# Performance work log

Hardware: AMD Instinct MI355X
Metric: run time of the kernel (lower is better)

## Reference

```python
import jax, jax.numpy as jnp
import numpy as np

N_NODES = 100000
N_EDGES = 3200000
D_IN = 128
D_OUT = 128


def setup_inputs() -> dict:
    key = jax.random.key(0)
    k1, k2, k3 = jax.random.split(key, 3)
    x = jax.random.normal(k1, (N_NODES, D_IN), dtype=jnp.float32)
    edge_index = jax.random.randint(k2, (2, N_EDGES), 0, N_NODES, dtype=jnp.int64)
    # Glorot-style init for GCN weight
    W = jax.random.normal(k3, (D_IN, D_OUT), dtype=jnp.float32) * (1.0 / np.sqrt(D_IN))
    b = jnp.zeros((D_OUT,), dtype=jnp.float32)
    return {"x": x, "edge_index": edge_index, "W": W, "b": b}


def reference(x, edge_index, W, b):
    # GCNConv (PyG semantics): add self-loops, symmetric normalization
    # D^-1/2 A D^-1/2, linear transform, aggregate, add bias; then ReLU.
    N = x.shape[0]
    loops = jnp.arange(N, dtype=edge_index.dtype)
    row = jnp.concatenate([edge_index[0], loops])  # source nodes
    col = jnp.concatenate([edge_index[1], loops])  # target nodes
    # degree over targets, with self-loop weight 1
    deg = jax.ops.segment_sum(jnp.ones_like(col, dtype=x.dtype), col,
                              num_segments=N)
    dinv = jnp.where(deg > 0, 1.0 / jnp.sqrt(deg), 0.0)
    norm = dinv[row] * dinv[col]                   # [E+N]
    xl = x @ W                                     # [N, D_OUT] dense GEMM
    msgs = xl[row] * norm[:, None]                 # gather + scale  [E+N, D_OUT]
    agg = jax.ops.segment_sum(msgs, col, num_segments=N)  # scatter-add
    return jax.nn.relu(agg + b)
```

## Files before the change

### kernel.cpp

```cpp
#include <hip/hip_runtime.h>
#include <hip/hip_bf16.h>
#include <math.h>

#define DF 128
#define TILE_EDGES 16384
#define NPB 256
#define NB_MAX 512

typedef __hip_bfloat16 bf16;
typedef __hip_bfloat162 bf16x2;

__global__ __launch_bounds__(1024) void k_binc(const int* __restrict__ col,
                                               int* __restrict__ counts,
                                               int E, int T, int NB) {
    __shared__ int h[NB_MAX];
    int tid = threadIdx.x;
    for (int i = tid; i < NB; i += 1024) h[i] = 0;
    __syncthreads();
    int tileBase = blockIdx.x * TILE_EDGES;
    for (int j = 0; j < TILE_EDGES / 1024; ++j) {
        int e = tileBase + j * 1024 + tid;
        if (e < E) atomicAdd(&h[col[e] >> 8], 1);
    }
    __syncthreads();
    for (int b = tid; b < NB; b += 1024)
        counts[b * T + blockIdx.x] = h[b];
}

__global__ __launch_bounds__(256) void k_scanA(int* __restrict__ data,
                                               int* __restrict__ blockSums, int M) {
    __shared__ int tmp[256];
    int tid = threadIdx.x;
    int n = blockIdx.x * 256 + tid;
    int v = (n < M) ? data[n] : 0;
    tmp[tid] = v;
    __syncthreads();
    for (int off = 1; off < 256; off <<= 1) {
        int t = (tid >= off) ? tmp[tid - off] : 0;
        __syncthreads();
        tmp[tid] += t;
        __syncthreads();
    }
    if (tid == 255) blockSums[blockIdx.x] = tmp[255];
    if (n < M) data[n] = tmp[tid] - v;
}

__global__ __launch_bounds__(512) void k_scanB(int* __restrict__ blockSums, int nb) {
    __shared__ int tmp[512];
    int tid = threadIdx.x;
    int v = (tid < nb) ? blockSums[tid] : 0;
    tmp[tid] = v;
    __syncthreads();
    for (int off = 1; off < 512; off <<= 1) {
        int t = (tid >= off) ? tmp[tid - off] : 0;
        __syncthreads();
        tmp[tid] += t;
        __syncthreads();
    }
    if (tid < nb) blockSums[tid] = tmp[tid] - v;
}

__global__ __launch_bounds__(256) void k_scanC(int* __restrict__ data,
                                               const int* __restrict__ blockSums,
                                               int* __restrict__ bucketBase,
                                               int M, int T, int NB, int E) {
    int n = blockIdx.x * 256 + threadIdx.x;
    if (n >= M) return;
    int v = data[n] + blockSums[n >> 8];
    data[n] = v;
    if (n % T == 0) bucketBase[n / T] = v;
    if (n == 0) bucketBase[NB] = E;
}

__global__ __launch_bounds__(1024) void k_binscatter(const int* __restrict__ edge,
                                                     const int* __restrict__ tileOff,
                                                     unsigned* __restrict__ binned,
                                                     int E, int T, int NB) {
    __shared__ int cur[NB_MAX];
    int tid = threadIdx.x;
    int t = blockIdx.x;
    for (int b = tid; b < NB; b += 1024) cur[b] = tileOff[b * T + t];
    __syncthreads();
    int tileBase = t * TILE_EDGES;
    for (int j = 0; j < TILE_EDGES / 1024; ++j) {
        int e = tileBase + j * 1024 + tid;
        if (e < E) {
            int r = edge[e];
            int c = edge[E + e];
            int pos = atomicAdd(&cur[c >> 8], 1);
            binned[pos] = ((unsigned)(c & (NPB - 1)) << 24) | (unsigned)r;
        }
    }
}

__global__ __launch_bounds__(512) void k_bucket(const unsigned* __restrict__ binned,
                                                const int* __restrict__ bucketBase,
                                                int* __restrict__ ssrc,
                                                int* __restrict__ offsets,
                                                int* __restrict__ deg,
                                                float* __restrict__ dinv, int N) {
    __shared__ int h[NPB], sc[NPB], cur[NPB];
    int tid = threadIdx.x;
    int b = blockIdx.x;
    int base = bucketBase[b];
    int cnt = bucketBase[b + 1] - base;
    if (tid < NPB) h[tid] = 0;
    __syncthreads();
    for (int i = tid; i < cnt; i += 512)
        atomicAdd(&h[binned[base + i] >> 24], 1);
    __syncthreads();
    if (tid < NPB) sc[tid] = h[tid];
    __syncthreads();
    for (int off = 1; off < NPB; off <<= 1) {
        int tv = (tid >= off && tid < NPB) ? sc[tid - off] : 0;
        __syncthreads();
        if (tid < NPB) sc[tid] += tv;
        __syncthreads();
    }
    if (tid < NPB) {
        int excl = sc[tid] - h[tid];
        cur[tid] = base + excl;
        int node = b * NPB + tid;
        if (node < N) {
            offsets[node] = base + excl;
            deg[node] = h[tid];
            dinv[node] = rsqrtf((float)(h[tid] + 1));
        }
    }
    __syncthreads();
    for (int i = tid; i < cnt; i += 512) {
        unsigned v = binned[base + i];
        int pos = atomicAdd(&cur[v >> 24], 1);
        ssrc[pos] = (int)(v & 0xFFFFFFu);
    }
}

__device__ inline void fma4(float4& acc, const float4 xv, const float4 w0,
                            const float4 w1, const float4 w2, const float4 w3) {
    acc.x = fmaf(xv.x, w0.x, fmaf(xv.y, w1.x, fmaf(xv.z, w2.x, fmaf(xv.w, w3.x, acc.x))));
    acc.y = fmaf(xv.x, w0.y, fmaf(xv.y, w1.y, fmaf(xv.z, w2.y, fmaf(xv.w, w3.y, acc.y))));
    acc.z = fmaf(xv.x, w0.z, fmaf(xv.y, w1.z, fmaf(xv.z, w2.z, fmaf(xv.w, w3.z, acc.z))));
    acc.w = fmaf(xv.x, w0.w, fmaf(xv.y, w1.w, fmaf(xv.z, w2.w, fmaf(xv.w, w3.w, acc.w))));
}

__device__ inline uint2 pack_bf16x4(float4 a) {
    union { uint2 u; bf16x2 h[2]; } p;
    p.h[0] = __float22bfloat162_rn(make_float2(a.x, a.y));
    p.h[1] = __float22bfloat162_rn(make_float2(a.z, a.w));
    return p.u;
}

__global__ __launch_bounds__(256) void k_gemm(const float* __restrict__ x,
                                              const float* __restrict__ W,
                                              const float* __restrict__ dinv,
                                              bf16* __restrict__ y, int N) {
    __shared__ float Ws[DF * DF];
    for (int i = threadIdx.x; i < DF * DF / 4; i += 256)
        ((float4*)Ws)[i] = ((const float4*)W)[i];
    __syncthreads();

    const int fg = (threadIdx.x & 31) * 4;
    const int rl = (threadIdx.x >> 5) * 4;

    for (int rowBase = blockIdx.x * 32; rowBase < N; rowBase += gridDim.x * 32) {
        int r0 = rowBase + rl;
        int c0 = min(r0 + 0, N - 1), c1 = min(r0 + 1, N - 1);
        int c2 = min(r0 + 2, N - 1), c3 = min(r0 + 3, N - 1);
        const float4* x0 = (const float4*)(x + (size_t)c0 * DF);
        const float4* x1 = (const float4*)(x + (size_t)c1 * DF);
        const float4* x2 = (const float4*)(x + (size_t)c2 * DF);
        const float4* x3 = (const float4*)(x + (size_t)c3 * DF);
        float4 a0 = {0, 0, 0, 0}, a1 = {0, 0, 0, 0}, a2 = {0, 0, 0, 0}, a3 = {0, 0, 0, 0};
        for (int k4 = 0; k4 < DF / 4; ++k4) {
            float4 xv0 = x0[k4], xv1 = x1[k4], xv2 = x2[k4], xv3 = x3[k4];
            int k = k4 * 4;
            float4 w0 = *(const float4*)(Ws + (k + 0) * DF + fg);
            float4 w1 = *(const float4*)(Ws + (k + 1) * DF + fg);
            float4 w2 = *(const float4*)(Ws + (k + 2) * DF + fg);
            float4 w3 = *(const float4*)(Ws + (k + 3) * DF + fg);
            fma4(a0, xv0, w0, w1, w2, w3);
            fma4(a1, xv1, w0, w1, w2, w3);
            fma4(a2, xv2, w0, w1, w2, w3);
            fma4(a3, xv3, w0, w1, w2, w3);
        }
        float d0 = dinv[c0], d1 = dinv[c1], d2 = dinv[c2], d3 = dinv[c3];
        a0.x *= d0; a0.y *= d0; a0.z *= d0; a0.w *= d0;
        a1.x *= d1; a1.y *= d1; a1.z *= d1; a1.w *= d1;
        a2.x *= d2; a2.y *= d2; a2.z *= d2; a2.w *= d2;
        a3.x *= d3; a3.y *= d3; a3.z *= d3; a3.w *= d3;
        if (r0 + 0 < N) *(uint2*)(y + (size_t)(r0 + 0) * DF + fg) = pack_bf16x4(a0);
        if (r0 + 1 < N) *(uint2*)(y + (size_t)(r0 + 1) * DF + fg) = pack_bf16x4(a1);
        if (r0 + 2 < N) *(uint2*)(y + (size_t)(r0 + 2) * DF + fg) = pack_bf16x4(a2);
        if (r0 + 3 < N) *(uint2*)(y + (size_t)(r0 + 3) * DF + fg) = pack_bf16x4(a3);
    }
}

__global__ __launch_bounds__(256) void k_gather(const bf16x2* __restrict__ y,
                                                const int* __restrict__ ssrc,
                                                const int* __restrict__ offsets,
                                                const int* __restrict__ deg,
                                                const float* __restrict__ dinv,
                                                const float* __restrict__ b,
                                                float* __restrict__ out, int N) {
    int wave = (blockIdx.x * 256 + threadIdx.x) >> 6;
    int lane = threadIdx.x & 63;
    if (wave >= N) return;
    int c = wave;
    int start = offsets[c];
    int d = deg[c];

    float2 acc = __bfloat1622float2(y[(size_t)c * 64 + lane]);

    for (int base = 0; base < d; base += 64) {
        int nb = min(64, d - base);
        int idx = ssrc[start + base + min(lane, nb - 1)];
        int j = 0;
        for (; j + 8 <= nb; j += 8) {
            int r0 = __shfl(idx, j + 0);
            int r1 = __shfl(idx, j + 1);
            int r2 = __shfl(idx, j + 2);
            int r3 = __shfl(idx, j + 3);
            int r4 = __shfl(idx, j + 4);
            int r5 = __shfl(idx, j + 5);
            int r6 = __shfl(idx, j + 6);
            int r7 = __shfl(idx, j + 7);
            float2 v0 = __bfloat1622float2(y[(size_t)r0 * 64 + lane]);
            float2 v1 = __bfloat1622float2(y[(size_t)r1 * 64 + lane]);
            float2 v2 = __bfloat1622float2(y[(size_t)r2 * 64 + lane]);
            float2 v3 = __bfloat1622float2(y[(size_t)r3 * 64 + lane]);
            float2 v4 = __bfloat1622float2(y[(size_t)r4 * 64 + lane]);
            float2 v5 = __bfloat1622float2(y[(size_t)r5 * 64 + lane]);
            float2 v6 = __bfloat1622float2(y[(size_t)r6 * 64 + lane]);
            float2 v7 = __bfloat1622float2(y[(size_t)r7 * 64 + lane]);
            acc.x += ((v0.x + v1.x) + (v2.x + v3.x)) + ((v4.x + v5.x) + (v6.x + v7.x));
            acc.y += ((v0.y + v1.y) + (v2.y + v3.y)) + ((v4.y + v5.y) + (v6.y + v7.y));
        }
        for (; j < nb; ++j) {
            int r = __shfl(idx, j);
            float2 v = __bfloat1622float2(y[(size_t)r * 64 + lane]);
            acc.x += v.x;
            acc.y += v.y;
        }
    }

    float dv = dinv[c];
    float2 bb = *(const float2*)(b + lane * 2);
    float2 o;
    o.x = fmaxf(fmaf(dv, acc.x, bb.x), 0.0f);
    o.y = fmaxf(fmaf(dv, acc.y, bb.y), 0.0f);
    *(float2*)(out + (size_t)c * DF + lane * 2) = o;
}

extern "C" void kernel_launch(void* const* d_in, const int* in_sizes, int n_in,
                              void* d_out, int out_size, void* d_ws, size_t ws_size,
                              hipStream_t stream) {
    const float* x    = (const float*)d_in[0];
    const int*   edge = (const int*)d_in[1];
    const float* W    = (const float*)d_in[2];
    const float* b    = (const float*)d_in[3];
    float*       out  = (float*)d_out;

    const int N = in_sizes[0] / DF;
    const int E = in_sizes[1] / 2;

    const int T  = (E + TILE_EDGES - 1) / TILE_EDGES;
    const int NB = (N + NPB - 1) / NPB;
    const int M  = NB * T;

    bf16*     y          = (bf16*)d_ws;
    int*      deg        = (int*)(y + (size_t)N * DF);
    float*    dinv       = (float*)(deg + N);
    int*      offsets    = (int*)(dinv + N);
    int*      bucketBase = offsets + N;
    int*      blockSums  = bucketBase + NB + 8;
    int*      counts     = blockSums + 512;
    unsigned* binned     = (unsigned*)(counts + M);
    int*      ssrc       = (int*)(binned + E);

    const int nbM = (M + 255) / 256;

    k_binc<<<T, 1024, 0, stream>>>(edge + E, counts, E, T, NB);
    k_scanA<<<nbM, 256, 0, stream>>>(counts, blockSums, M);
    k_scanB<<<1, 512, 0, stream>>>(blockSums, nbM);
    k_scanC<<<nbM, 256, 0, stream>>>(counts, blockSums, bucketBase, M, T, NB, E);
    k_binscatter<<<T, 1024, 0, stream>>>(edge, counts, binned, E, T, NB);
    k_bucket<<<NB, 512, 0, stream>>>(binned, bucketBase, ssrc, offsets, deg, dinv, N);
    k_gemm<<<(N + 31) / 32, 256, 0, stream>>>(x, W, dinv, y, N);
    k_gather<<<(N + 3) / 4, 256, 0, stream>>>((const bf16x2*)y, ssrc, offsets, deg, dinv, b, out, N);
}
```

Before: 374.6 us.

## Use bf16 MFMA for the feature GEMM and shrink binning tiles

Replaces the fp32 FMA GEMM with bf16 MFMA 16x16x32 instructions. W is stored transposed in bf16 in padded LDS, and x rows are converted to bf16 on load. Separately, the edge-binning tile size drops to 6144 edges with 512-thread blocks, which gives more blocks for the count and scatter passes. The scan kernels are widened to 1024 so they can handle the larger number of tile-bucket counters. The input activations are now rounded to bf16, and y stores become scalar bf16 writes rather than packed vectors.

```diff
diff --git a/kernel.cpp b/kernel.cpp
--- a/kernel.cpp
+++ b/kernel.cpp
@@ -3,27 +3,35 @@
 #include <math.h>
 
 #define DF 128
-#define TILE_EDGES 16384
+#define TILE_EDGES 6144
 #define NPB 256
 #define NB_MAX 512
+#define KP 136
 
 typedef __hip_bfloat16 bf16;
 typedef __hip_bfloat162 bf16x2;
-
-__global__ __launch_bounds__(1024) void k_binc(const int* __restrict__ col,
-                                               int* __restrict__ counts,
-                                               int E, int T, int NB) {
+typedef __attribute__((ext_vector_type(8))) short short8;
+typedef __attribute__((ext_vector_type(4))) float f32x4;
+
+__device__ inline short bf16bits(float f) {
+    __hip_bfloat16 h = __float2bfloat16(f);
+    return *reinterpret_cast<short*>(&h);
+}
+
+__global__ __launch_bounds__(512) void k_binc(const int* __restrict__ col,
+                                              int* __restrict__ counts,
+                                              int E, int T, int NB) {
     __shared__ int h[NB_MAX];
     int tid = threadIdx.x;
-    for (int i = tid; i < NB; i += 1024) h[i] = 0;
+    for (int i = tid; i < NB; i += 512) h[i] = 0;
     __syncthreads();
     int tileBase = blockIdx.x * TILE_EDGES;
-    for (int j = 0; j < TILE_EDGES / 1024; ++j) {
-        int e = tileBase + j * 1024 + tid;
+    for (int j = 0; j < TILE_EDGES / 512; ++j) {
+        int e = tileBase + j * 512 + tid;
         if (e < E) atomicAdd(&h[col[e] >> 8], 1);
     }
     __syncthreads();
-    for (int b = tid; b < NB; b += 1024)
+    for (int b = tid; b < NB; b += 512)
         counts[b * T + blockIdx.x] = h[b];
 }
 
@@ -45,13 +53,13 @@
     if (n < M) data[n] = tmp[tid] - v;
 }
 
-__global__ __launch_bounds__(512) void k_scanB(int* __restrict__ blockSums, int nb) {
-    __shared__ int tmp[512];
+__global__ __launch_bounds__(1024) void k_scanB(int* __restrict__ blockSums, int nb) {
+    __shared__ int tmp[1024];
     int tid = threadIdx.x;
     int v = (tid < nb) ? blockSums[tid] : 0;
     tmp[tid] = v;
     __syncthreads();
-    for (int off = 1; off < 512; off <<= 1) {
+    for (int off = 1; off < 1024; off <<= 1) {
         int t = (tid >= off) ? tmp[tid - off] : 0;
         __syncthreads();
         tmp[tid] += t;
@@ -72,18 +80,18 @@
     if (n == 0) bucketBase[NB] = E;
 }
 
-__global__ __launch_bounds__(1024) void k_binscatter(const int* __restrict__ edge,
-                                                     const int* __restrict__ tileOff,
-                                                     unsigned* __restrict__ binned,
-                                                     int E, int T, int NB) {
+__global__ __launch_bounds__(512) void k_binscatter(const int* __restrict__ edge,
+                                                    const int* __restrict__ tileOff,
+                                                    unsigned* __restrict__ binned,
+                                                    int E, int T, int NB) {
     __shared__ int cur[NB_MAX];
     int tid = threadIdx.x;
     int t = blockIdx.x;
-    for (int b = tid; b < NB; b += 1024) cur[b] = tileOff[b * T + t];
+    for (int b = tid; b < NB; b += 512) cur[b] = tileOff[b * T + t];
     __syncthreads();
     int tileBase = t * TILE_EDGES;
-    for (int j = 0; j < TILE_EDGES / 1024; ++j) {
-        int e = tileBase + j * 1024 + tid;
+    for (int j = 0; j < TILE_EDGES / 512; ++j) {
+        int e = tileBase + j * 512 + tid;
         if (e < E) {
             int r = edge[e];
             int c = edge[E + e];
@@ -135,63 +143,61 @@
     }
 }
 
-__device__ inline void fma4(float4& acc, const float4 xv, const float4 w0,
-                            const float4 w1, const float4 w2, const float4 w3) {
-    acc.x = fmaf(xv.x, w0.x, fmaf(xv.y, w1.x, fmaf(xv.z, w2.x, fmaf(xv.w, w3.x, acc.x))));
-    acc.y = fmaf(xv.x, w0.y, fmaf(xv.y, w1.y, fmaf(xv.z, w2.y, fmaf(xv.w, w3.y, acc.y))));
-    acc.z = fmaf(xv.x, w0.z, fmaf(xv.y, w1.z, fmaf(xv.z, w2.z, fmaf(xv.w, w3.z, acc.z))));
-    acc.w = fmaf(xv.x, w0.w, fmaf(xv.y, w1.w, fmaf(xv.z, w2.w, fmaf(xv.w, w3.w, acc.w))));
-}
-
-__device__ inline uint2 pack_bf16x4(float4 a) {
-    union { uint2 u; bf16x2 h[2]; } p;
-    p.h[0] = __float22bfloat162_rn(make_float2(a.x, a.y));
-    p.h[1] = __float22bfloat162_rn(make_float2(a.z, a.w));
-    return p.u;
-}
-
 __global__ __launch_bounds__(256) void k_gemm(const float* __restrict__ x,
                                               const float* __restrict__ W,
                                               const float* __restrict__ dinv,
                                               bf16* __restrict__ y, int N) {
-    __shared__ float Ws[DF * DF];
-    for (int i = threadIdx.x; i < DF * DF / 4; i += 256)
-        ((float4*)Ws)[i] = ((const float4*)W)[i];
-    __syncthreads();
-
-    const int fg = (threadIdx.x & 31) * 4;
-    const int rl = (threadIdx.x >> 5) * 4;
-
-    for (int rowBase = blockIdx.x * 32; rowBase < N; rowBase += gridDim.x * 32) {
-        int r0 = rowBase + rl;
-        int c0 = min(r0 + 0, N - 1), c1 = min(r0 + 1, N - 1);
-        int c2 = min(r0 + 2, N - 1), c3 = min(r0 + 3, N - 1);
-        const float4* x0 = (const float4*)(x + (size_t)c0 * DF);
-        const float4* x1 = (const float4*)(x + (size_t)c1 * DF);
-        const float4* x2 = (const float4*)(x + (size_t)c2 * DF);
-        const float4* x3 = (const float4*)(x + (size_t)c3 * DF);
-        float4 a0 = {0, 0, 0, 0}, a1 = {0, 0, 0, 0}, a2 = {0, 0, 0, 0}, a3 = {0, 0, 0, 0};
-        for (int k4 = 0; k4 < DF / 4; ++k4) {
-            float4 xv0 = x0[k4], xv1 = x1[k4], xv2 = x2[k4], xv3 = x3[k4];
-            int k = k4 * 4;
-            float4 w0 = *(const float4*)(Ws + (k + 0) * DF + fg);
-            float4 w1 = *(const float4*)(Ws + (k + 1) * DF + fg);
-            float4 w2 = *(const float4*)(Ws + (k + 2) * DF + fg);
-            float4 w3 = *(const float4*)(Ws + (k + 3) * DF + fg);
-            fma4(a0, xv0, w0, w1, w2, w3);
-            fma4(a1, xv1, w0, w1, w2, w3);
-            fma4(a2, xv2, w0, w1, w2, w3);
-            fma4(a3, xv3, w0, w1, w2, w3);
-        }
-        float d0 = dinv[c0], d1 = dinv[c1], d2 = dinv[c2], d3 = dinv[c3];
-        a0.x *= d0; a0.y *= d0; a0.z *= d0; a0.w *= d0;
-        a1.x *= d1; a1.y *= d1; a1.z *= d1; a1.w *= d1;
-        a2.x *= d2; a2.y *= d2; a2.z *= d2; a2.w *= d2;
-        a3.x *= d3; a3.y *= d3; a3.z *= d3; a3.w *= d3;
-        if (r0 + 0 < N) *(uint2*)(y + (size_t)(r0 + 0) * DF + fg) = pack_bf16x4(a0);
-        if (r0 + 1 < N) *(uint2*)(y + (size_t)(r0 + 1) * DF + fg) = pack_bf16x4(a1);
-        if (r0 + 2 < N) *(uint2*)(y + (size_t)(r0 + 2) * DF + fg) = pack_bf16x4(a2);
-        if (r0 + 3 < N) *(uint2*)(y + (size_t)(r0 + 3) * DF + fg) = pack_bf16x4(a3);
+    __shared__ bf16 Wt[DF * KP];
+    int tid = threadIdx.x;
+    for (int i = tid; i < DF * (DF / 4); i += 256) {
+        int k = i >> 5;
+        int n4 = (i & 31) * 4;
+        float4 w = *(const float4*)(W + k * DF + n4);
+        Wt[(n4 + 0) * KP + k] = __float2bfloat16(w.x);
+        Wt[(n4 + 1) * KP + k] = __float2bfloat16(w.y);
+        Wt[(n4 + 2) * KP + k] = __float2bfloat16(w.z);
+        Wt[(n4 + 3) * KP + k] = __float2bfloat16(w.w);
+    }
+    __syncthreads();
+
+    const int wv = tid >> 6;
+    const int lane = tid & 63;
+    const int m16 = lane & 15;
+    const int q = lane >> 4;
+    const int rbase = blockIdx.x * 64 + wv * 16;
+    const int arow = min(rbase + m16, N - 1);
+
+    f32x4 acc[8];
+#pragma unroll
+    for (int nt = 0; nt < 8; ++nt) acc[nt] = (f32x4){0.f, 0.f, 0.f, 0.f};
+
+#pragma unroll
+    for (int kc = 0; kc < 4; ++kc) {
+        int k0 = kc * 32 + q * 8;
+        float4 xa = *(const float4*)(x + (size_t)arow * DF + k0);
+        float4 xb = *(const float4*)(x + (size_t)arow * DF + k0 + 4);
+        short8 a;
+        a[0] = bf16bits(xa.x); a[1] = bf16bits(xa.y);
+        a[2] = bf16bits(xa.z); a[3] = bf16bits(xa.w);
+        a[4] = bf16bits(xb.x); a[5] = bf16bits(xb.y);
+        a[6] = bf16bits(xb.z); a[7] = bf16bits(xb.w);
+#pragma unroll
+        for (int nt = 0; nt < 8; ++nt) {
+            short8 b = *(const short8*)(Wt + (nt * 16 + m16) * KP + k0);
+            acc[nt] = __builtin_amdgcn_mfma_f32_16x16x32_bf16(a, b, acc[nt], 0, 0, 0);
+        }
+    }
+
+#pragma unroll
+    for (int r = 0; r < 4; ++r) {
+        int orow = rbase + q * 4 + r;
+        if (orow < N) {
+            float dv = dinv[orow];
+#pragma unroll
+            for (int nt = 0; nt < 8; ++nt) {
+                y[(size_t)orow * DF + nt * 16 + m16] = __float2bfloat16(acc[nt][r] * dv);
+            }
+        }
     }
 }
 
@@ -273,18 +279,18 @@
     int*      offsets    = (int*)(dinv + N);
     int*      bucketBase = offsets + N;
     int*      blockSums  = bucketBase + NB + 8;
-    int*      counts     = blockSums + 512;
+    int*      counts     = blockSums + 1024;
     unsigned* binned     = (unsigned*)(counts + M);
     int*      ssrc       = (int*)(binned + E);
 
     const int nbM = (M + 255) / 256;
 
-    k_binc<<<T, 1024, 0, stream>>>(edge + E, counts, E, T, NB);
+    k_binc<<<T, 512, 0, stream>>>(edge + E, counts, E, T, NB);
     k_scanA<<<nbM, 256, 0, stream>>>(counts, blockSums, M);
-    k_scanB<<<1, 512, 0, stream>>>(blockSums, nbM);
+    k_scanB<<<1, 1024, 0, stream>>>(blockSums, nbM);
     k_scanC<<<nbM, 256, 0, stream>>>(counts, blockSums, bucketBase, M, T, NB, E);
-    k_binscatter<<<T, 1024, 0, stream>>>(edge, counts, binned, E, T, NB);
+    k_binscatter<<<T, 512, 0, stream>>>(edge, counts, binned, E, T, NB);
     k_bucket<<<NB, 512, 0, stream>>>(binned, bucketBase, ssrc, offsets, deg, dinv, N);
-    k_gemm<<<(N + 31) / 32, 256, 0, stream>>>(x, W, dinv, y, N);
+    k_gemm<<<(N + 63) / 64, 256, 0, stream>>>(x, W, dinv, y, N);
     k_gather<<<(N + 3) / 4, 256, 0, stream>>>((const bf16x2*)y, ssrc, offsets, deg, dinv, b, out, N);
 }
```

New measurement: 324.5 us. -13.4%, faster.
